# Kernel tuning notes

Hardware: AMD Instinct MI355X
Metric: run time of the kernel (lower is better)

## Reference

```python
import jax, jax.numpy as jnp
import numpy as np

N_NODES = 100000
N_EDGES = 1600000
N_FEAT = 128
HIDDEN = 128
N_GRAPHS = 100


def setup_inputs() -> dict:
    key = jax.random.key(0)
    ks = jax.random.split(key, 12)
    glorot = lambda k, fi, fo: jax.random.normal(k, (fo, fi), jnp.float32) * (1.0 / np.sqrt(fi))
    x = jax.random.normal(ks[0], (N_NODES, N_FEAT), jnp.float32)
    edge_index = jax.random.randint(ks[1], (2, N_EDGES), 0, N_NODES, jnp.int64)
    batch = jnp.sort(jax.random.randint(ks[2], (N_NODES,), 0, N_GRAPHS, jnp.int64))
    return {
        "x": x,
        "edge_index": edge_index,
        "batch": batch,
        "W1": glorot(ks[3], N_FEAT, HIDDEN), "b1": jnp.zeros((HIDDEN,), jnp.float32),
        "W2": glorot(ks[4], HIDDEN, HIDDEN), "b2": jnp.zeros((HIDDEN,), jnp.float32),
        "W3": glorot(ks[5], HIDDEN, HIDDEN), "b3": jnp.zeros((HIDDEN,), jnp.float32),
        "W4": glorot(ks[6], HIDDEN, HIDDEN), "b4": jnp.zeros((HIDDEN,), jnp.float32),
    }


def _aggregate(x, edge_index):
    # GIN aggregation with eps=0: (1+eps)*x_i + sum_{j in N(i)} x_j
    src, dst = edge_index[0], edge_index[1]
    agg = jax.ops.segment_sum(x[src], dst, num_segments=N_NODES)
    return x + agg


def _mlp(h, Wa, ba, Wb, bb):
    h = jax.nn.relu(h @ Wa.T + ba)
    return jax.nn.relu(h @ Wb.T + bb)


def reference(x, edge_index, batch, W1, b1, W2, b2, W3, b3, W4, b4):
    # conv1: GINConv(MLP1), then extra relu (no-op after MLP's relu), dropout in eval = identity
    h = _mlp(_aggregate(x, edge_index), W1, b1, W2, b2)
    # conv2: GINConv(MLP2), then relu
    h = _mlp(_aggregate(h, edge_index), W3, b3, W4, b4)
    # global mean pool over graphs
    sums = jax.ops.segment_sum(h, batch, num_segments=N_GRAPHS)
    counts = jax.ops.segment_sum(jnp.ones((h.shape[0],), h.dtype), batch, num_segments=N_GRAPHS)
    x_pool = sums / jnp.maximum(counts, 1.0)[:, None]
    return (x_pool, h)
```

## Files before the change

kernel.cpp:

```cpp
#include <hip/hip_runtime.h>

#define N_NODES  100000
#define N_EDGES  1600000
#define NF       128
#define N_GRAPHS 100
#define NBKT     391
#define BKT_SHIFT 8
#define CAP      6144
#define CAPN     48
#define EPB      4096
#define EB_GRID  391

typedef __attribute__((ext_vector_type(8))) short bf16x8;
typedef __attribute__((ext_vector_type(4))) float f32x4;
typedef __attribute__((ext_vector_type(2))) float f32x2;
typedef unsigned int uint32;

__device__ __forceinline__ unsigned short f2bf(float f) {
    union { float f; uint32 u; } x; x.f = f;
    return (unsigned short)((x.u + 0x7fffu + ((x.u >> 16) & 1u)) >> 16);
}
__device__ __forceinline__ uint32 pack2bf(float a, float b) {
    union { float f; uint32 u; } x, y; x.f = a; y.f = b;
    uint32 lo = (x.u + 0x7fffu + ((x.u >> 16) & 1u)) >> 16;
    uint32 hi = (y.u + 0x7fffu + ((y.u >> 16) & 1u)) & 0xffff0000u;
    return lo | hi;
}
__device__ __forceinline__ void add8(f32x2* acc, uint4 u4) {
    uint32 u[4] = {u4.x, u4.y, u4.z, u4.w};
    #pragma unroll
    for (int i = 0; i < 4; ++i) {
        union { uint32 b; float f; } lo, hi;
        lo.b = u[i] << 16; hi.b = u[i] & 0xffff0000u;
        acc[i] += (f32x2){lo.f, hi.f};
    }
}

__global__ __launch_bounds__(256) void prep(const float4* __restrict__ x,
                                            const float4* __restrict__ w1,
                                            const float4* __restrict__ w2,
                                            const float4* __restrict__ w3,
                                            const float4* __restrict__ w4,
                                            uint4* __restrict__ xb, uint4* __restrict__ wb,
                                            int* __restrict__ cur, float* __restrict__ sums) {
    int bid = blockIdx.x, t = threadIdx.x;
    if (bid < 6250) {
        int i = bid * 256 + t;
        float4 a = x[i * 2], b = x[i * 2 + 1];
        uint4 o;
        o.x = pack2bf(a.x, a.y); o.y = pack2bf(a.z, a.w);
        o.z = pack2bf(b.x, b.y); o.w = pack2bf(b.z, b.w);
        xb[i] = o;
    } else if (bid < 6282) {
        int i = (bid - 6250) * 256 + t;
        int wi = i >> 11, li = i & 2047;
        const float4* s = (wi == 0) ? w1 : (wi == 1) ? w2 : (wi == 2) ? w3 : w4;
        float4 a = s[li * 2], b = s[li * 2 + 1];
        uint4 o;
        o.x = pack2bf(a.x, a.y); o.y = pack2bf(a.z, a.w);
        o.z = pack2bf(b.x, b.y); o.w = pack2bf(b.z, b.w);
        wb[i] = o;
    } else {
        int idx = (bid - 6282) * 256 + t;
        for (int i = idx; i < N_GRAPHS * NF; i += 4096) sums[i] = 0.f;
        if (idx < NBKT) cur[idx] = 0;
    }
}

__global__ __launch_bounds__(512) void bscatter(const int* __restrict__ src,
                                                const int* __restrict__ dst,
                                                int* __restrict__ cur,
                                                uint32* __restrict__ ebuf) {
    __shared__ int lh[NBKT], lbase[NBKT];
    int t = threadIdx.x;
    if (t < NBKT) lh[t] = 0;
    __syncthreads();
    int e0 = blockIdx.x * EPB;
    int d[8];
    #pragma unroll
    for (int i = 0; i < 8; ++i) {
        int e = e0 + i * 512 + t;
        d[i] = -1;
        if (e < N_EDGES) { d[i] = dst[e]; atomicAdd(&lh[d[i] >> BKT_SHIFT], 1); }
    }
    __syncthreads();
    if (t < NBKT) { lbase[t] = t * CAP + atomicAdd(&cur[t], lh[t]); lh[t] = 0; }
    __syncthreads();
    #pragma unroll
    for (int i = 0; i < 8; ++i) {
        int e = e0 + i * 512 + t;
        if (e < N_EDGES) {
            int b = d[i] >> BKT_SHIFT;
            int off = atomicAdd(&lh[b], 1);
            ebuf[lbase[b] + off] = ((uint32)(d[i] & 255) << 17) | (uint32)src[e];
        }
    }
}

__global__ __launch_bounds__(256) void bfine(const uint32* __restrict__ ebuf,
                                             const int* __restrict__ cur,
                                             int* __restrict__ cnt,
                                             int* __restrict__ csr) {
    __shared__ int off[256];
    int t = threadIdx.x;
    int bkt = blockIdx.x;
    int beg = bkt * CAP;
    int end = beg + cur[bkt];
    off[t] = 0;
    __syncthreads();
    for (int e = beg + t; e < end; e += 256) {
        uint32 u = ebuf[e];
        int local = (int)(u >> 17);
        int pos = atomicAdd(&off[local], 1);
        if (pos < CAPN)
            csr[((bkt << BKT_SHIFT) + local) * CAPN + pos] = (int)(u & 0x1FFFFu);
    }
    __syncthreads();
    int node = (bkt << BKT_SHIFT) + t;
    if (node < N_NODES) cnt[node] = min(off[t], CAPN);
}

__global__ __launch_bounds__(256) void gather_agg_bf16(const uint4* __restrict__ x,
                                                       const int* __restrict__ cnt,
                                                       const int* __restrict__ csr,
                                                       uint4* __restrict__ out) {
    int gid  = blockIdx.x * 256 + threadIdx.x;
    int node = gid >> 6;
    int l = threadIdx.x & 63;
    int c = l & 15;
    int j = l >> 4;
    int beg = node * CAPN;

    uint4 vself = x[(size_t)node * 16 + c];
    int myE = csr[beg + min(l, CAPN - 1)];
    int deg = cnt[node];

    f32x2 acc[4];
    #pragma unroll
    for (int i = 0; i < 4; ++i) acc[i] = (f32x2){0.f, 0.f};

    uint4 v[8];
    int ok[8];
    #pragma unroll
    for (int k = 0; k < 4; ++k) {
        int sl = j + 4 * k;
        int sle = max(min(sl, deg - 1), 0);
        unsigned s = (unsigned)__shfl(myE, sle, 64);
        s = min(s, (unsigned)(N_NODES - 1));
        v[k] = x[(size_t)s * 16 + c];
        ok[k] = sl < deg;
    }
    if (deg > 16) {
        #pragma unroll
        for (int k = 0; k < 4; ++k) {
            int sl = 16 + j + 4 * k;
            int sle = min(sl, deg - 1);
            unsigned s = (unsigned)__shfl(myE, sle, 64);
            s = min(s, (unsigned)(N_NODES - 1));
            v[4 + k] = x[(size_t)s * 16 + c];
            ok[4 + k] = sl < deg;
        }
    }
    #pragma unroll
    for (int k = 0; k < 4; ++k) if (ok[k]) add8(acc, v[k]);
    if (deg > 16) {
        #pragma unroll
        for (int k = 0; k < 4; ++k) if (ok[4 + k]) add8(acc, v[4 + k]);
        for (int sl0 = 32; sl0 < deg; sl0 += 16) {
            #pragma unroll
            for (int k = 0; k < 4; ++k) {
                int sl = sl0 + j + 4 * k;
                int sle = min(sl, deg - 1);
                unsigned s = (unsigned)__shfl(myE, sle, 64);
                s = min(s, (unsigned)(N_NODES - 1));
                uint4 vv = x[(size_t)s * 16 + c];
                if (sl < deg) add8(acc, vv);
            }
        }
    }

    #pragma unroll
    for (int i = 0; i < 4; ++i) {
        acc[i].x += __shfl_xor(acc[i].x, 16, 64);
        acc[i].y += __shfl_xor(acc[i].y, 16, 64);
        acc[i].x += __shfl_xor(acc[i].x, 32, 64);
        acc[i].y += __shfl_xor(acc[i].y, 32, 64);
    }

    add8(acc, vself);

    if (j == 0) {
        uint4 o;
        o.x = pack2bf(acc[0].x, acc[0].y); o.y = pack2bf(acc[1].x, acc[1].y);
        o.z = pack2bf(acc[2].x, acc[2].y); o.w = pack2bf(acc[3].x, acc[3].y);
        out[(size_t)node * 16 + c] = o;
    }
}

template <bool F32OUT>
__global__ __launch_bounds__(256, 4) void mlp_mfma(const unsigned short* __restrict__ A,
                                                   const unsigned short* __restrict__ Wa,
                                                   const float* __restrict__ ba,
                                                   const unsigned short* __restrict__ Wb,
                                                   const float* __restrict__ bb,
                                                   void* __restrict__ Cout, int M) {
    __shared__ unsigned short Mid[128 * 136];
    int tid  = threadIdx.x;
    int row0 = blockIdx.x * 128;
    int wv = tid >> 6, l = tid & 63, lm = l & 15, q = l >> 4;

    const unsigned short* pa0 = A + (size_t)min(row0 + wv * 32 + lm,      M - 1) * NF;
    const unsigned short* pa1 = A + (size_t)min(row0 + wv * 32 + 16 + lm, M - 1) * NF;
    const unsigned short* pwa = Wa + lm * NF;
    const unsigned short* pwb = Wb + lm * NF;

    f32x4 acc[2][8];
    #pragma unroll
    for (int i = 0; i < 2; ++i)
        #pragma unroll
        for (int j = 0; j < 8; ++j) acc[i][j] = (f32x4){0.f, 0.f, 0.f, 0.f};

    #pragma unroll
    for (int ks = 0; ks < 4; ++ks) {
        int ko = ks * 32 + q * 8;
        bf16x8 a0 = *(const bf16x8*)(pa0 + ko);
        bf16x8 a1 = *(const bf16x8*)(pa1 + ko);
        #pragma unroll
        for (int ct = 0; ct < 8; ++ct) {
            bf16x8 b = *(const bf16x8*)(pwa + ct * 16 * NF + ko);
            acc[0][ct] = __builtin_amdgcn_mfma_f32_16x16x32_bf16(a0, b, acc[0][ct], 0, 0, 0);
            acc[1][ct] = __builtin_amdgcn_mfma_f32_16x16x32_bf16(a1, b, acc[1][ct], 0, 0, 0);
        }
    }

    #pragma unroll
    for (int rt = 0; rt < 2; ++rt)
        #pragma unroll
        for (int ct = 0; ct < 8; ++ct) {
            int col = ct * 16 + lm;
            float bv = ba[col];
            #pragma unroll
            for (int r = 0; r < 4; ++r) {
                int rr = wv * 32 + rt * 16 + q * 4 + r;
                Mid[rr * 136 + col] = f2bf(fmaxf(acc[rt][ct][r] + bv, 0.f));
            }
        }
    __syncthreads();

    #pragma unroll
    for (int i = 0; i < 2; ++i)
        #pragma unroll
        for (int j = 0; j < 8; ++j) acc[i][j] = (f32x4){0.f, 0.f, 0.f, 0.f};

    const unsigned short* pm0 = &Mid[(wv * 32 + lm) * 136];
    const unsigned short* pm1 = &Mid[(wv * 32 + 16 + lm) * 136];
    #pragma unroll
    for (int ks = 0; ks < 4; ++ks) {
        int ko = ks * 32 + q * 8;
        bf16x8 a0 = *(const bf16x8*)(pm0 + ko);
        bf16x8 a1 = *(const bf16x8*)(pm1 + ko);
        #pragma unroll
        for (int ct = 0; ct < 8; ++ct) {
            bf16x8 b = *(const bf16x8*)(pwb + ct * 16 * NF + ko);
            acc[0][ct] = __builtin_amdgcn_mfma_f32_16x16x32_bf16(a0, b, acc[0][ct], 0, 0, 0);
            acc[1][ct] = __builtin_amdgcn_mfma_f32_16x16x32_bf16(a1, b, acc[1][ct], 0, 0, 0);
        }
    }

    #pragma unroll
    for (int rt = 0; rt < 2; ++rt)
        #pragma unroll
        for (int ct = 0; ct < 8; ++ct) {
            int col = ct * 16 + lm;
            float bv = bb[col];
            #pragma unroll
            for (int r = 0; r < 4; ++r) {
                int row = row0 + wv * 32 + rt * 16 + q * 4 + r;
                if (row < M) {
                    float v = fmaxf(acc[rt][ct][r] + bv, 0.f);
                    if (F32OUT) ((float*)Cout)[(size_t)row * NF + col] = v;
                    else ((unsigned short*)Cout)[(size_t)row * NF + col] = f2bf(v);
                }
            }
        }
}

__global__ __launch_bounds__(256) void pool_sum2(const float* __restrict__ h,
                                                 const int* __restrict__ batch,
                                                 float* __restrict__ sums) {
    int t = threadIdx.x;
    int f = t & 127, seg = t >> 7;
    int n0 = blockIdx.x * 128 + seg * 64;
    if (n0 >= N_NODES) return;
    int n1 = min(n0 + 64, N_NODES);
    int cur = batch[n0];
    float acc = 0.f;
    for (int n = n0; n < n1; ++n) {
        int g = batch[n];
        if (g != cur) {
            atomicAdd(&sums[cur * NF + f], acc);
            acc = 0.f; cur = g;
        }
        acc += h[(size_t)n * NF + f];
    }
    atomicAdd(&sums[cur * NF + f], acc);
}

__global__ __launch_bounds__(256) void pool_div2(const float* __restrict__ sums,
                                                 const int* __restrict__ batch,
                                                 float* __restrict__ out) {
    int i = blockIdx.x * 256 + threadIdx.x;
    if (i >= N_GRAPHS * NF) return;
    int g = i >> 7;
    int lo = 0, hi = N_NODES;
    while (lo < hi) { int m = (lo + hi) >> 1; if (batch[m] < g) lo = m + 1; else hi = m; }
    int lo2 = lo, hi2 = N_NODES;
    while (lo2 < hi2) { int m = (lo2 + hi2) >> 1; if (batch[m] < g + 1) lo2 = m + 1; else hi2 = m; }
    float cnt = (float)(lo2 - lo);
    out[i] = sums[i] / fmaxf(cnt, 1.f);
}

extern "C" void kernel_launch(void* const* d_in, const int* in_sizes, int n_in,
                              void* d_out, int out_size, void* d_ws, size_t ws_size,
                              hipStream_t stream) {
    const float* x     = (const float*)d_in[0];
    const int*   ei    = (const int*)d_in[1];
    const int*   batch = (const int*)d_in[2];
    const float* W1 = (const float*)d_in[3];  const float* b1 = (const float*)d_in[4];
    const float* W2 = (const float*)d_in[5];  const float* b2 = (const float*)d_in[6];
    const float* W3 = (const float*)d_in[7];  const float* b3 = (const float*)d_in[8];
    const float* W4 = (const float*)d_in[9];  const float* b4 = (const float*)d_in[10];
    const int* src = ei;
    const int* dst = ei + N_EDGES;

    float* out   = (float*)d_out;
    float* h_out = out + N_GRAPHS * NF;

    const size_t NE = (size_t)N_NODES * NF;
    unsigned short* xb = (unsigned short*)d_ws;
    unsigned short* t0 = xb + NE;
    unsigned short* t1 = t0 + NE;
    unsigned short* Wb = t1 + NE;
    int*    csr  = (int*)(Wb + 4 * NF * NF);
    int*    cntp = csr + (size_t)N_NODES * CAPN;
    int*    curp = cntp + N_NODES;
    float*  sums = (float*)(curp + NBKT);
    uint32* ebuf = (uint32*)t1;

    const int gather_blocks = N_NODES * 64 / 256;
    const int gemm_blocks   = (N_NODES + 127) / 128;

    prep<<<6250 + 32 + 16, 256, 0, stream>>>((const float4*)x,
                                             (const float4*)W1, (const float4*)W2,
                                             (const float4*)W3, (const float4*)W4,
                                             (uint4*)xb, (uint4*)Wb, curp, sums);

    bscatter<<<EB_GRID, 512, 0, stream>>>(src, dst, curp, ebuf);
    bfine<<<NBKT, 256, 0, stream>>>(ebuf, curp, cntp, csr);

    gather_agg_bf16<<<gather_blocks, 256, 0, stream>>>((const uint4*)xb, cntp, csr, (uint4*)t0);
    mlp_mfma<false><<<gemm_blocks, 256, 0, stream>>>(t0, Wb + 0 * NF * NF, b1,
                                                     Wb + 1 * NF * NF, b2, t1, N_NODES);

    gather_agg_bf16<<<gather_blocks, 256, 0, stream>>>((const uint4*)t1, cntp, csr, (uint4*)t0);
    mlp_mfma<true ><<<gemm_blocks, 256, 0, stream>>>(t0, Wb + 2 * NF * NF, b3,
                                                     Wb + 3 * NF * NF, b4, h_out, N_NODES);

    pool_sum2<<<(N_NODES + 127) / 128, 256, 0, stream>>>(h_out, batch, sums);
    pool_div2<<<(N_GRAPHS * NF + 255) / 256, 256, 0, stream>>>(sums, batch, out);
}
```

Measured before the change: 394.7 us.

## Use persistent gather waves with prefetch and spread edge bucketing over more blocks

The gather kernel becomes persistent: a fixed grid of waves loops over nodes and prefetches the next node's CSR row and degree while the current node's neighbours are summed. The edge bucketing now uses smaller blocks (1024 edges each, so more blocks) and skips global atomics for empty buckets. The fine pass splits each bucket across four blocks and uses global atomics on per-node counters, which are now zeroed in prep, instead of a shared-memory histogram. This raises parallelism in the CSR build at the cost of more global atomic traffic. Degrees are clamped to CAPN when read in the gather.

New measurement: 473.9 us. 1.2x slower.

```diff
diff --git a/kernel.cpp b/kernel.cpp
--- a/kernel.cpp
+++ b/kernel.cpp
@@ -8,8 +8,10 @@
 #define BKT_SHIFT 8
 #define CAP      6144
 #define CAPN     48
-#define EPB      4096
-#define EB_GRID  391
+#define EPB      1024
+#define EB_GRID  1563
+#define GBLOCKS  2048
+#define NWAVES   (GBLOCKS * 4)
 
 typedef __attribute__((ext_vector_type(8))) short bf16x8;
 typedef __attribute__((ext_vector_type(4))) float f32x4;
@@ -42,7 +44,8 @@
                                             const float4* __restrict__ w3,
                                             const float4* __restrict__ w4,
                                             uint4* __restrict__ xb, uint4* __restrict__ wb,
-                                            int* __restrict__ cur, float* __restrict__ sums) {
+                                            int* __restrict__ cur, int* __restrict__ cnt,
+                                            float* __restrict__ sums) {
     int bid = blockIdx.x, t = threadIdx.x;
     if (bid < 6250) {
         int i = bid * 256 + t;
@@ -62,33 +65,38 @@
         wb[i] = o;
     } else {
         int idx = (bid - 6282) * 256 + t;
-        for (int i = idx; i < N_GRAPHS * NF; i += 4096) sums[i] = 0.f;
+        for (int i = idx; i < N_NODES; i += 8192) cnt[i] = 0;
+        for (int i = idx; i < N_GRAPHS * NF; i += 8192) sums[i] = 0.f;
         if (idx < NBKT) cur[idx] = 0;
     }
 }
 
-__global__ __launch_bounds__(512) void bscatter(const int* __restrict__ src,
+__global__ __launch_bounds__(256) void bscatter(const int* __restrict__ src,
                                                 const int* __restrict__ dst,
                                                 int* __restrict__ cur,
                                                 uint32* __restrict__ ebuf) {
     __shared__ int lh[NBKT], lbase[NBKT];
     int t = threadIdx.x;
-    if (t < NBKT) lh[t] = 0;
+    for (int i = t; i < NBKT; i += 256) lh[i] = 0;
     __syncthreads();
     int e0 = blockIdx.x * EPB;
-    int d[8];
-    #pragma unroll
-    for (int i = 0; i < 8; ++i) {
-        int e = e0 + i * 512 + t;
+    int d[4];
+    #pragma unroll
+    for (int i = 0; i < 4; ++i) {
+        int e = e0 + i * 256 + t;
         d[i] = -1;
         if (e < N_EDGES) { d[i] = dst[e]; atomicAdd(&lh[d[i] >> BKT_SHIFT], 1); }
     }
     __syncthreads();
-    if (t < NBKT) { lbase[t] = t * CAP + atomicAdd(&cur[t], lh[t]); lh[t] = 0; }
+    for (int i = t; i < NBKT; i += 256) {
+        int h = lh[i];
+        lbase[i] = i * CAP + (h ? atomicAdd(&cur[i], h) : 0);
+        lh[i] = 0;
+    }
     __syncthreads();
     #pragma unroll
-    for (int i = 0; i < 8; ++i) {
-        int e = e0 + i * 512 + t;
+    for (int i = 0; i < 4; ++i) {
+        int e = e0 + i * 256 + t;
         if (e < N_EDGES) {
             int b = d[i] >> BKT_SHIFT;
             int off = atomicAdd(&lh[b], 1);
@@ -101,99 +109,106 @@
                                              const int* __restrict__ cur,
                                              int* __restrict__ cnt,
                                              int* __restrict__ csr) {
-    __shared__ int off[256];
-    int t = threadIdx.x;
-    int bkt = blockIdx.x;
+    int bkt = blockIdx.x >> 2, q = blockIdx.x & 3;
     int beg = bkt * CAP;
-    int end = beg + cur[bkt];
-    off[t] = 0;
-    __syncthreads();
-    for (int e = beg + t; e < end; e += 256) {
+    int end = beg + min(cur[bkt], CAP);
+    int lo = beg + q * (CAP / 4);
+    int hi = min(lo + (CAP / 4), end);
+    for (int e = lo + (int)threadIdx.x; e < hi; e += 256) {
         uint32 u = ebuf[e];
-        int local = (int)(u >> 17);
-        int pos = atomicAdd(&off[local], 1);
+        int node = (bkt << BKT_SHIFT) + (int)(u >> 17);
+        int pos = atomicAdd(&cnt[node], 1);
         if (pos < CAPN)
-            csr[((bkt << BKT_SHIFT) + local) * CAPN + pos] = (int)(u & 0x1FFFFu);
-    }
-    __syncthreads();
-    int node = (bkt << BKT_SHIFT) + t;
-    if (node < N_NODES) cnt[node] = min(off[t], CAPN);
+            csr[node * CAPN + pos] = (int)(u & 0x1FFFFu);
+    }
 }
 
 __global__ __launch_bounds__(256) void gather_agg_bf16(const uint4* __restrict__ x,
                                                        const int* __restrict__ cnt,
                                                        const int* __restrict__ csr,
                                                        uint4* __restrict__ out) {
-    int gid  = blockIdx.x * 256 + threadIdx.x;
-    int node = gid >> 6;
+    int wid = (blockIdx.x * 256 + threadIdx.x) >> 6;
     int l = threadIdx.x & 63;
     int c = l & 15;
     int j = l >> 4;
-    int beg = node * CAPN;
-
-    uint4 vself = x[(size_t)node * 16 + c];
-    int myE = csr[beg + min(l, CAPN - 1)];
-    int deg = cnt[node];
-
-    f32x2 acc[4];
-    #pragma unroll
-    for (int i = 0; i < 4; ++i) acc[i] = (f32x2){0.f, 0.f};
-
-    uint4 v[8];
-    int ok[8];
-    #pragma unroll
-    for (int k = 0; k < 4; ++k) {
-        int sl = j + 4 * k;
-        int sle = max(min(sl, deg - 1), 0);
-        unsigned s = (unsigned)__shfl(myE, sle, 64);
-        s = min(s, (unsigned)(N_NODES - 1));
-        v[k] = x[(size_t)s * 16 + c];
-        ok[k] = sl < deg;
-    }
-    if (deg > 16) {
+    int le = min(l, CAPN - 1);
+
+    int node = wid;
+    int E  = csr[node * CAPN + le];
+    int dg = cnt[node];
+
+    while (node < N_NODES) {
+        int nn = node + NWAVES;
+        int deg = min(dg, CAPN);
+
+        uint4 vself = x[(size_t)node * 16 + c];
+
+        uint4 v[8];
         #pragma unroll
         for (int k = 0; k < 4; ++k) {
-            int sl = 16 + j + 4 * k;
-            int sle = min(sl, deg - 1);
-            unsigned s = (unsigned)__shfl(myE, sle, 64);
+            int sl = j + 4 * k;
+            int sle = max(min(sl, deg - 1), 0);
+            unsigned s = (unsigned)__shfl(E, sle, 64);
             s = min(s, (unsigned)(N_NODES - 1));
-            v[4 + k] = x[(size_t)s * 16 + c];
-            ok[4 + k] = sl < deg;
-        }
-    }
-    #pragma unroll
-    for (int k = 0; k < 4; ++k) if (ok[k]) add8(acc, v[k]);
-    if (deg > 16) {
-        #pragma unroll
-        for (int k = 0; k < 4; ++k) if (ok[4 + k]) add8(acc, v[4 + k]);
-        for (int sl0 = 32; sl0 < deg; sl0 += 16) {
+            v[k] = x[(size_t)s * 16 + c];
+        }
+        if (deg > 16) {
             #pragma unroll
             for (int k = 0; k < 4; ++k) {
-                int sl = sl0 + j + 4 * k;
+                int sl = 16 + j + 4 * k;
                 int sle = min(sl, deg - 1);
-                unsigned s = (unsigned)__shfl(myE, sle, 64);
+                unsigned s = (unsigned)__shfl(E, sle, 64);
                 s = min(s, (unsigned)(N_NODES - 1));
-                uint4 vv = x[(size_t)s * 16 + c];
-                if (sl < deg) add8(acc, vv);
+                v[4 + k] = x[(size_t)s * 16 + c];
             }
         }
-    }
-
-    #pragma unroll
-    for (int i = 0; i < 4; ++i) {
-        acc[i].x += __shfl_xor(acc[i].x, 16, 64);
-        acc[i].y += __shfl_xor(acc[i].y, 16, 64);
-        acc[i].x += __shfl_xor(acc[i].x, 32, 64);
-        acc[i].y += __shfl_xor(acc[i].y, 32, 64);
-    }
-
-    add8(acc, vself);
-
-    if (j == 0) {
-        uint4 o;
-        o.x = pack2bf(acc[0].x, acc[0].y); o.y = pack2bf(acc[1].x, acc[1].y);
-        o.z = pack2bf(acc[2].x, acc[2].y); o.w = pack2bf(acc[3].x, acc[3].y);
-        out[(size_t)node * 16 + c] = o;
+
+        int En = 0, dgn = 0;
+        if (nn < N_NODES) {
+            En  = csr[nn * CAPN + le];
+            dgn = cnt[nn];
+        }
+
+        f32x2 acc[4];
+        #pragma unroll
+        for (int i = 0; i < 4; ++i) acc[i] = (f32x2){0.f, 0.f};
+
+        #pragma unroll
+        for (int k = 0; k < 4; ++k) if (j + 4 * k < deg) add8(acc, v[k]);
+        if (deg > 16) {
+            #pragma unroll
+            for (int k = 0; k < 4; ++k) if (16 + j + 4 * k < deg) add8(acc, v[4 + k]);
+            for (int sl0 = 32; sl0 < deg; sl0 += 16) {
+                #pragma unroll
+                for (int k = 0; k < 4; ++k) {
+                    int sl = sl0 + j + 4 * k;
+                    int sle = min(sl, deg - 1);
+                    unsigned s = (unsigned)__shfl(E, sle, 64);
+                    s = min(s, (unsigned)(N_NODES - 1));
+                    uint4 vv = x[(size_t)s * 16 + c];
+                    if (sl < deg) add8(acc, vv);
+                }
+            }
+        }
+
+        #pragma unroll
+        for (int i = 0; i < 4; ++i) {
+            acc[i].x += __shfl_xor(acc[i].x, 16, 64);
+            acc[i].y += __shfl_xor(acc[i].y, 16, 64);
+            acc[i].x += __shfl_xor(acc[i].x, 32, 64);
+            acc[i].y += __shfl_xor(acc[i].y, 32, 64);
+        }
+
+        add8(acc, vself);
+
+        if (j == 0) {
+            uint4 o;
+            o.x = pack2bf(acc[0].x, acc[0].y); o.y = pack2bf(acc[1].x, acc[1].y);
+            o.z = pack2bf(acc[2].x, acc[2].y); o.w = pack2bf(acc[3].x, acc[3].y);
+            out[(size_t)node * 16 + c] = o;
+        }
+
+        node = nn; E = En; dg = dgn;
     }
 }
 
@@ -347,22 +362,21 @@
     float*  sums = (float*)(curp + NBKT);
     uint32* ebuf = (uint32*)t1;
 
-    const int gather_blocks = N_NODES * 64 / 256;
-    const int gemm_blocks   = (N_NODES + 127) / 128;
-
-    prep<<<6250 + 32 + 16, 256, 0, stream>>>((const float4*)x,
+    const int gemm_blocks = (N_NODES + 127) / 128;
+
+    prep<<<6250 + 32 + 32, 256, 0, stream>>>((const float4*)x,
                                              (const float4*)W1, (const float4*)W2,
                                              (const float4*)W3, (const float4*)W4,
-                                             (uint4*)xb, (uint4*)Wb, curp, sums);
-
-    bscatter<<<EB_GRID, 512, 0, stream>>>(src, dst, curp, ebuf);
-    bfine<<<NBKT, 256, 0, stream>>>(ebuf, curp, cntp, csr);
-
-    gather_agg_bf16<<<gather_blocks, 256, 0, stream>>>((const uint4*)xb, cntp, csr, (uint4*)t0);
+                                             (uint4*)xb, (uint4*)Wb, curp, cntp, sums);
+
+    bscatter<<<EB_GRID, 256, 0, stream>>>(src, dst, curp, ebuf);
+    bfine<<<NBKT * 4, 256, 0, stream>>>(ebuf, curp, cntp, csr);
+
+    gather_agg_bf16<<<GBLOCKS, 256, 0, stream>>>((const uint4*)xb, cntp, csr, (uint4*)t0);
     mlp_mfma<false><<<gemm_blocks, 256, 0, stream>>>(t0, Wb + 0 * NF * NF, b1,
                                                      Wb + 1 * NF * NF, b2, t1, N_NODES);
 
-    gather_agg_bf16<<<gather_blocks, 256, 0, stream>>>((const uint4*)t1, cntp, csr, (uint4*)t0);
+    gather_agg_bf16<<<GBLOCKS, 256, 0, stream>>>((const uint4*)t1, cntp, csr, (uint4*)t0);
     mlp_mfma<true ><<<gemm_blocks, 256, 0, stream>>>(t0, Wb + 2 * NF * NF, b3,
                                                      Wb + 3 * NF * NF, b4, h_out, N_NODES);
 
```

## Split gather/MLP stages so MLP on first part overlaps gather of remainder

Applied to the files above, without the earlier changes.

Each GIN layer's gather and MLP are split at a node boundary. The first gather covers the first part of the nodes. A fused kernel then runs MLP blocks on that part alongside gather blocks for the rest, and a final MLP launch finishes the tail, so compute-bound GEMM overlaps memory-bound gather. bfine also stages its CSR rows in shared memory and writes them out as coalesced uint4 copies, and pool_sum now uses float4 loads. The cost is a large shared-memory buffer in bfine that lowers its occupancy, plus an extra kernel launch per layer.

Result: slower. 404.4 us (+2.5%).

```diff
diff --git a/kernel.cpp b/kernel.cpp
--- a/kernel.cpp
+++ b/kernel.cpp
@@ -10,6 +10,12 @@
 #define CAPN     48
 #define EPB      4096
 #define EB_GRID  391
+#define HSPLIT   66560
+#define MBLK_A   520
+#define GNODES_B (N_NODES - HSPLIT)
+#define GBLK_B   (GNODES_B / 4)
+#define GBLK_A   (HSPLIT / 4)
+#define MBLK_B   262
 
 typedef __attribute__((ext_vector_type(8))) short bf16x8;
 typedef __attribute__((ext_vector_type(4))) float f32x4;
@@ -102,10 +108,11 @@
                                              int* __restrict__ cnt,
                                              int* __restrict__ csr) {
     __shared__ int off[256];
+    __shared__ __align__(16) int lcsr[256 * CAPN];
     int t = threadIdx.x;
     int bkt = blockIdx.x;
     int beg = bkt * CAP;
-    int end = beg + cur[bkt];
+    int end = beg + min(cur[bkt], CAP);
     off[t] = 0;
     __syncthreads();
     for (int e = beg + t; e < end; e += 256) {
@@ -113,22 +120,22 @@
         int local = (int)(u >> 17);
         int pos = atomicAdd(&off[local], 1);
         if (pos < CAPN)
-            csr[((bkt << BKT_SHIFT) + local) * CAPN + pos] = (int)(u & 0x1FFFFu);
+            lcsr[local * CAPN + pos] = (int)(u & 0x1FFFFu);
     }
     __syncthreads();
     int node = (bkt << BKT_SHIFT) + t;
     if (node < N_NODES) cnt[node] = min(off[t], CAPN);
-}
-
-__global__ __launch_bounds__(256) void gather_agg_bf16(const uint4* __restrict__ x,
-                                                       const int* __restrict__ cnt,
-                                                       const int* __restrict__ csr,
-                                                       uint4* __restrict__ out) {
-    int gid  = blockIdx.x * 256 + threadIdx.x;
-    int node = gid >> 6;
-    int l = threadIdx.x & 63;
-    int c = l & 15;
-    int j = l >> 4;
+    uint4* dstq = (uint4*)(csr + (size_t)bkt * 256 * CAPN);
+    const uint4* srcq = (const uint4*)lcsr;
+    for (int i = t; i < 256 * CAPN / 4; i += 256)
+        dstq[i] = srcq[i];
+}
+
+__device__ __forceinline__ void gather_one(const uint4* __restrict__ x,
+                                           const int* __restrict__ cnt,
+                                           const int* __restrict__ csr,
+                                           uint4* __restrict__ out,
+                                           int node, int l, int c, int j) {
     int beg = node * CAPN;
 
     uint4 vself = x[(size_t)node * 16 + c];
@@ -197,16 +204,26 @@
     }
 }
 
+__global__ __launch_bounds__(256) void gather_agg_bf16(const uint4* __restrict__ x,
+                                                       const int* __restrict__ cnt,
+                                                       const int* __restrict__ csr,
+                                                       uint4* __restrict__ out,
+                                                       int g0) {
+    int gid  = blockIdx.x * 256 + threadIdx.x;
+    int node = g0 + (gid >> 6);
+    int l = threadIdx.x & 63;
+    gather_one(x, cnt, csr, out, node, l, l & 15, l >> 4);
+}
+
 template <bool F32OUT>
-__global__ __launch_bounds__(256, 4) void mlp_mfma(const unsigned short* __restrict__ A,
-                                                   const unsigned short* __restrict__ Wa,
-                                                   const float* __restrict__ ba,
-                                                   const unsigned short* __restrict__ Wb,
-                                                   const float* __restrict__ bb,
-                                                   void* __restrict__ Cout, int M) {
+__device__ __forceinline__ void mlp_body(const unsigned short* __restrict__ A,
+                                         const unsigned short* __restrict__ Wa,
+                                         const float* __restrict__ ba,
+                                         const unsigned short* __restrict__ Wb,
+                                         const float* __restrict__ bb,
+                                         void* __restrict__ Cout, int M, int row0) {
     __shared__ unsigned short Mid[128 * 136];
     int tid  = threadIdx.x;
-    int row0 = blockIdx.x * 128;
     int wv = tid >> 6, l = tid & 63, lm = l & 15, q = l >> 4;
 
     const unsigned short* pa0 = A + (size_t)min(row0 + wv * 32 + lm,      M - 1) * NF;
@@ -285,25 +302,63 @@
         }
 }
 
-__global__ __launch_bounds__(256) void pool_sum2(const float* __restrict__ h,
+template <bool F32OUT>
+__global__ __launch_bounds__(256, 4) void mlp_mfma(const unsigned short* __restrict__ A,
+                                                   const unsigned short* __restrict__ Wa,
+                                                   const float* __restrict__ ba,
+                                                   const unsigned short* __restrict__ Wb,
+                                                   const float* __restrict__ bb,
+                                                   void* __restrict__ Cout, int M, int rowBase) {
+    mlp_body<F32OUT>(A, Wa, ba, Wb, bb, Cout, M, rowBase + blockIdx.x * 128);
+}
+
+template <bool F32OUT>
+__global__ __launch_bounds__(256, 4) void fused_mg(const unsigned short* __restrict__ A,
+                                                   const unsigned short* __restrict__ Wa,
+                                                   const float* __restrict__ ba,
+                                                   const unsigned short* __restrict__ Wb,
+                                                   const float* __restrict__ bb,
+                                                   void* __restrict__ Cout,
+                                                   const uint4* __restrict__ gx,
+                                                   const int* __restrict__ cnt,
+                                                   const int* __restrict__ csr,
+                                                   uint4* __restrict__ gout) {
+    if (blockIdx.x < MBLK_A) {
+        mlp_body<F32OUT>(A, Wa, ba, Wb, bb, Cout, HSPLIT, blockIdx.x * 128);
+    } else {
+        int idx = (blockIdx.x - MBLK_A) * 256 + threadIdx.x;
+        int node = HSPLIT + (idx >> 6);
+        int l = threadIdx.x & 63;
+        gather_one(gx, cnt, csr, gout, node, l, l & 15, l >> 4);
+    }
+}
+
+__global__ __launch_bounds__(256) void pool_sum4(const float4* __restrict__ h,
                                                  const int* __restrict__ batch,
                                                  float* __restrict__ sums) {
     int t = threadIdx.x;
-    int f = t & 127, seg = t >> 7;
-    int n0 = blockIdx.x * 128 + seg * 64;
+    int f4 = t & 31, seg = t >> 5;
+    int n0 = blockIdx.x * 512 + seg * 64;
     if (n0 >= N_NODES) return;
     int n1 = min(n0 + 64, N_NODES);
     int cur = batch[n0];
-    float acc = 0.f;
+    float4 acc = {0.f, 0.f, 0.f, 0.f};
     for (int n = n0; n < n1; ++n) {
         int g = batch[n];
         if (g != cur) {
-            atomicAdd(&sums[cur * NF + f], acc);
-            acc = 0.f; cur = g;
-        }
-        acc += h[(size_t)n * NF + f];
-    }
-    atomicAdd(&sums[cur * NF + f], acc);
+            atomicAdd(&sums[cur * NF + f4 * 4 + 0], acc.x);
+            atomicAdd(&sums[cur * NF + f4 * 4 + 1], acc.y);
+            atomicAdd(&sums[cur * NF + f4 * 4 + 2], acc.z);
+            atomicAdd(&sums[cur * NF + f4 * 4 + 3], acc.w);
+            acc = (float4){0.f, 0.f, 0.f, 0.f}; cur = g;
+        }
+        float4 v = h[(size_t)n * 32 + f4];
+        acc.x += v.x; acc.y += v.y; acc.z += v.z; acc.w += v.w;
+    }
+    atomicAdd(&sums[cur * NF + f4 * 4 + 0], acc.x);
+    atomicAdd(&sums[cur * NF + f4 * 4 + 1], acc.y);
+    atomicAdd(&sums[cur * NF + f4 * 4 + 2], acc.z);
+    atomicAdd(&sums[cur * NF + f4 * 4 + 3], acc.w);
 }
 
 __global__ __launch_bounds__(256) void pool_div2(const float* __restrict__ sums,
@@ -337,18 +392,16 @@
     float* h_out = out + N_GRAPHS * NF;
 
     const size_t NE = (size_t)N_NODES * NF;
+    const size_t CSRSZ = (size_t)NBKT * 256 * CAPN;
     unsigned short* xb = (unsigned short*)d_ws;
     unsigned short* t0 = xb + NE;
     unsigned short* t1 = t0 + NE;
     unsigned short* Wb = t1 + NE;
     int*    csr  = (int*)(Wb + 4 * NF * NF);
-    int*    cntp = csr + (size_t)N_NODES * CAPN;
+    int*    cntp = csr + CSRSZ;
     int*    curp = cntp + N_NODES;
     float*  sums = (float*)(curp + NBKT);
     uint32* ebuf = (uint32*)t1;
-
-    const int gather_blocks = N_NODES * 64 / 256;
-    const int gemm_blocks   = (N_NODES + 127) / 128;
 
     prep<<<6250 + 32 + 16, 256, 0, stream>>>((const float4*)x,
                                              (const float4*)W1, (const float4*)W2,
@@ -358,14 +411,20 @@
     bscatter<<<EB_GRID, 512, 0, stream>>>(src, dst, curp, ebuf);
     bfine<<<NBKT, 256, 0, stream>>>(ebuf, curp, cntp, csr);
 
-    gather_agg_bf16<<<gather_blocks, 256, 0, stream>>>((const uint4*)xb, cntp, csr, (uint4*)t0);
-    mlp_mfma<false><<<gemm_blocks, 256, 0, stream>>>(t0, Wb + 0 * NF * NF, b1,
-                                                     Wb + 1 * NF * NF, b2, t1, N_NODES);
-
-    gather_agg_bf16<<<gather_blocks, 256, 0, stream>>>((const uint4*)t1, cntp, csr, (uint4*)t0);
-    mlp_mfma<true ><<<gemm_blocks, 256, 0, stream>>>(t0, Wb + 2 * NF * NF, b3,
-                                                     Wb + 3 * NF * NF, b4, h_out, N_NODES);
-
-    pool_sum2<<<(N_NODES + 127) / 128, 256, 0, stream>>>(h_out, batch, sums);
+    gather_agg_bf16<<<GBLK_A, 256, 0, stream>>>((const uint4*)xb, cntp, csr, (uint4*)t0, 0);
+    fused_mg<false><<<MBLK_A + GBLK_B, 256, 0, stream>>>(t0, Wb + 0 * NF * NF, b1,
+                                                         Wb + 1 * NF * NF, b2, t1,
+                                                         (const uint4*)xb, cntp, csr, (uint4*)t0);
+    mlp_mfma<false><<<MBLK_B, 256, 0, stream>>>(t0, Wb + 0 * NF * NF, b1,
+                                                Wb + 1 * NF * NF, b2, t1, N_NODES, HSPLIT);
+
+    gather_agg_bf16<<<GBLK_A, 256, 0, stream>>>((const uint4*)t1, cntp, csr, (uint4*)t0, 0);
+    fused_mg<true ><<<MBLK_A + GBLK_B, 256, 0, stream>>>(t0, Wb + 2 * NF * NF, b3,
+                                                         Wb + 3 * NF * NF, b4, h_out,
+                                                         (const uint4*)t1, cntp, csr, (uint4*)t0);
+    mlp_mfma<true ><<<MBLK_B, 256, 0, stream>>>(t0, Wb + 2 * NF * NF, b3,
+                                                Wb + 3 * NF * NF, b4, h_out, N_NODES, HSPLIT);
+
+    pool_sum4<<<(N_NODES + 511) / 512, 256, 0, stream>>>((const float4*)h_out, batch, sums);
     pool_div2<<<(N_GRAPHS * NF + 255) / 256, 256, 0, stream>>>(sums, batch, out);
 }
```

## Fuse neighbor gather with MFMA MLP and stage CSR build in LDS

Applied to the files above, without the earlier changes.

Replaces the separate gather-aggregate and MLP kernels with one 512-thread kernel per 128-row tile. It aggregates neighbor features straight into LDS and runs both MFMA GEMMs from there. This removes the bf16 intermediate buffer round trip through global memory and one launch per layer. It also builds each bucket's CSR in LDS before a coalesced copy-out, skips zero-count global atomics in bscatter, and vectorizes the pool sum with float4. The cost is less parallelism in the gather, since each wave walks 16 nodes serially, plus higher LDS use per block, which may lower occupancy and latency hiding for the random loads.

Result: slower. 467.3 us (+18.4%).

```diff
diff --git a/kernel.cpp b/kernel.cpp
--- a/kernel.cpp
+++ b/kernel.cpp
@@ -10,6 +10,7 @@
 #define CAPN     48
 #define EPB      4096
 #define EB_GRID  391
+#define FBLOCKS  782
 
 typedef __attribute__((ext_vector_type(8))) short bf16x8;
 typedef __attribute__((ext_vector_type(4))) float f32x4;
@@ -84,7 +85,7 @@
         if (e < N_EDGES) { d[i] = dst[e]; atomicAdd(&lh[d[i] >> BKT_SHIFT], 1); }
     }
     __syncthreads();
-    if (t < NBKT) { lbase[t] = t * CAP + atomicAdd(&cur[t], lh[t]); lh[t] = 0; }
+    if (t < NBKT) { lbase[t] = t * CAP + (lh[t] ? atomicAdd(&cur[t], lh[t]) : 0); lh[t] = 0; }
     __syncthreads();
     #pragma unroll
     for (int i = 0; i < 8; ++i) {
@@ -102,10 +103,11 @@
                                              int* __restrict__ cnt,
                                              int* __restrict__ csr) {
     __shared__ int off[256];
+    __shared__ __align__(16) int lcsr[256 * CAPN];
     int t = threadIdx.x;
     int bkt = blockIdx.x;
     int beg = bkt * CAP;
-    int end = beg + cur[bkt];
+    int end = beg + min(cur[bkt], CAP);
     off[t] = 0;
     __syncthreads();
     for (int e = beg + t; e < end; e += 256) {
@@ -113,197 +115,195 @@
         int local = (int)(u >> 17);
         int pos = atomicAdd(&off[local], 1);
         if (pos < CAPN)
-            csr[((bkt << BKT_SHIFT) + local) * CAPN + pos] = (int)(u & 0x1FFFFu);
+            lcsr[local * CAPN + pos] = (int)(u & 0x1FFFFu);
     }
     __syncthreads();
     int node = (bkt << BKT_SHIFT) + t;
     if (node < N_NODES) cnt[node] = min(off[t], CAPN);
-}
-
-__global__ __launch_bounds__(256) void gather_agg_bf16(const uint4* __restrict__ x,
-                                                       const int* __restrict__ cnt,
-                                                       const int* __restrict__ csr,
-                                                       uint4* __restrict__ out) {
-    int gid  = blockIdx.x * 256 + threadIdx.x;
-    int node = gid >> 6;
-    int l = threadIdx.x & 63;
+    uint4* dstq = (uint4*)(csr + (size_t)bkt * 256 * CAPN);
+    const uint4* srcq = (const uint4*)lcsr;
+    for (int i = t; i < 256 * CAPN / 4; i += 256)
+        dstq[i] = srcq[i];
+}
+
+template <bool F32OUT>
+__global__ __launch_bounds__(512) void fused_gml(const uint4* __restrict__ x,
+                                                 const int* __restrict__ cnt,
+                                                 const int* __restrict__ csr,
+                                                 const unsigned short* __restrict__ Wa,
+                                                 const float* __restrict__ ba,
+                                                 const unsigned short* __restrict__ Wb,
+                                                 const float* __restrict__ bb,
+                                                 void* __restrict__ Cout) {
+    __shared__ __align__(16) unsigned short AM[128 * 136];
+    int tid = threadIdx.x;
+    int wv = tid >> 6;
+    int l  = tid & 63;
     int c = l & 15;
     int j = l >> 4;
-    int beg = node * CAPN;
-
-    uint4 vself = x[(size_t)node * 16 + c];
-    int myE = csr[beg + min(l, CAPN - 1)];
-    int deg = cnt[node];
-
-    f32x2 acc[4];
-    #pragma unroll
-    for (int i = 0; i < 4; ++i) acc[i] = (f32x2){0.f, 0.f};
-
-    uint4 v[8];
-    int ok[8];
-    #pragma unroll
-    for (int k = 0; k < 4; ++k) {
-        int sl = j + 4 * k;
-        int sle = max(min(sl, deg - 1), 0);
-        unsigned s = (unsigned)__shfl(myE, sle, 64);
-        s = min(s, (unsigned)(N_NODES - 1));
-        v[k] = x[(size_t)s * 16 + c];
-        ok[k] = sl < deg;
-    }
-    if (deg > 16) {
+    int row0 = blockIdx.x * 128;
+
+    for (int i = 0; i < 16; ++i) {
+        int lrow = wv * 16 + i;
+        int node = min(row0 + lrow, N_NODES - 1);
+        int beg = node * CAPN;
+
+        uint4 vself = x[(size_t)node * 16 + c];
+        int myE = csr[beg + min(l, CAPN - 1)];
+        int deg = cnt[node];
+
+        f32x2 acc[4];
+        #pragma unroll
+        for (int a = 0; a < 4; ++a) acc[a] = (f32x2){0.f, 0.f};
+
+        uint4 v[8];
+        int ok[8];
         #pragma unroll
         for (int k = 0; k < 4; ++k) {
-            int sl = 16 + j + 4 * k;
-            int sle = min(sl, deg - 1);
+            int sl = j + 4 * k;
+            int sle = max(min(sl, deg - 1), 0);
             unsigned s = (unsigned)__shfl(myE, sle, 64);
             s = min(s, (unsigned)(N_NODES - 1));
-            v[4 + k] = x[(size_t)s * 16 + c];
-            ok[4 + k] = sl < deg;
-        }
-    }
-    #pragma unroll
-    for (int k = 0; k < 4; ++k) if (ok[k]) add8(acc, v[k]);
-    if (deg > 16) {
-        #pragma unroll
-        for (int k = 0; k < 4; ++k) if (ok[4 + k]) add8(acc, v[4 + k]);
-        for (int sl0 = 32; sl0 < deg; sl0 += 16) {
+            v[k] = x[(size_t)s * 16 + c];
+            ok[k] = sl < deg;
+        }
+        if (deg > 16) {
             #pragma unroll
             for (int k = 0; k < 4; ++k) {
-                int sl = sl0 + j + 4 * k;
+                int sl = 16 + j + 4 * k;
                 int sle = min(sl, deg - 1);
                 unsigned s = (unsigned)__shfl(myE, sle, 64);
                 s = min(s, (unsigned)(N_NODES - 1));
-                uint4 vv = x[(size_t)s * 16 + c];
-                if (sl < deg) add8(acc, vv);
+                v[4 + k] = x[(size_t)s * 16 + c];
+                ok[4 + k] = sl < deg;
             }
         }
-    }
-
-    #pragma unroll
-    for (int i = 0; i < 4; ++i) {
-        acc[i].x += __shfl_xor(acc[i].x, 16, 64);
-        acc[i].y += __shfl_xor(acc[i].y, 16, 64);
-        acc[i].x += __shfl_xor(acc[i].x, 32, 64);
-        acc[i].y += __shfl_xor(acc[i].y, 32, 64);
-    }
-
-    add8(acc, vself);
-
-    if (j == 0) {
-        uint4 o;
-        o.x = pack2bf(acc[0].x, acc[0].y); o.y = pack2bf(acc[1].x, acc[1].y);
-        o.z = pack2bf(acc[2].x, acc[2].y); o.w = pack2bf(acc[3].x, acc[3].y);
-        out[(size_t)node * 16 + c] = o;
-    }
-}
-
-template <bool F32OUT>
-__global__ __launch_bounds__(256, 4) void mlp_mfma(const unsigned short* __restrict__ A,
-                                                   const unsigned short* __restrict__ Wa,
-                                                   const float* __restrict__ ba,
-                                                   const unsigned short* __restrict__ Wb,
-                                                   const float* __restrict__ bb,
-                                                   void* __restrict__ Cout, int M) {
-    __shared__ unsigned short Mid[128 * 136];
-    int tid  = threadIdx.x;
-    int row0 = blockIdx.x * 128;
-    int wv = tid >> 6, l = tid & 63, lm = l & 15, q = l >> 4;
-
-    const unsigned short* pa0 = A + (size_t)min(row0 + wv * 32 + lm,      M - 1) * NF;
-    const unsigned short* pa1 = A + (size_t)min(row0 + wv * 32 + 16 + lm, M - 1) * NF;
+        #pragma unroll
+        for (int k = 0; k < 4; ++k) if (ok[k]) add8(acc, v[k]);
+        if (deg > 16) {
+            #pragma unroll
+            for (int k = 0; k < 4; ++k) if (ok[4 + k]) add8(acc, v[4 + k]);
+            for (int sl0 = 32; sl0 < deg; sl0 += 16) {
+                #pragma unroll
+                for (int k = 0; k < 4; ++k) {
+                    int sl = sl0 + j + 4 * k;
+                    int sle = min(sl, deg - 1);
+                    unsigned s = (unsigned)__shfl(myE, sle, 64);
+                    s = min(s, (unsigned)(N_NODES - 1));
+                    uint4 vv = x[(size_t)s * 16 + c];
+                    if (sl < deg) add8(acc, vv);
+                }
+            }
+        }
+
+        #pragma unroll
+        for (int a = 0; a < 4; ++a) {
+            acc[a].x += __shfl_xor(acc[a].x, 16, 64);
+            acc[a].y += __shfl_xor(acc[a].y, 16, 64);
+            acc[a].x += __shfl_xor(acc[a].x, 32, 64);
+            acc[a].y += __shfl_xor(acc[a].y, 32, 64);
+        }
+
+        add8(acc, vself);
+
+        if (j == 0) {
+            uint4 o;
+            o.x = pack2bf(acc[0].x, acc[0].y); o.y = pack2bf(acc[1].x, acc[1].y);
+            o.z = pack2bf(acc[2].x, acc[2].y); o.w = pack2bf(acc[3].x, acc[3].y);
+            *(uint4*)&AM[lrow * 136 + c * 8] = o;
+        }
+    }
+    __syncthreads();
+
+    int lm = c, q = j;
+    const unsigned short* pa  = &AM[(wv * 16 + lm) * 136];
     const unsigned short* pwa = Wa + lm * NF;
     const unsigned short* pwb = Wb + lm * NF;
 
-    f32x4 acc[2][8];
-    #pragma unroll
-    for (int i = 0; i < 2; ++i)
-        #pragma unroll
-        for (int j = 0; j < 8; ++j) acc[i][j] = (f32x4){0.f, 0.f, 0.f, 0.f};
+    f32x4 acc[8];
+    #pragma unroll
+    for (int ct = 0; ct < 8; ++ct) acc[ct] = (f32x4){0.f, 0.f, 0.f, 0.f};
 
     #pragma unroll
     for (int ks = 0; ks < 4; ++ks) {
         int ko = ks * 32 + q * 8;
-        bf16x8 a0 = *(const bf16x8*)(pa0 + ko);
-        bf16x8 a1 = *(const bf16x8*)(pa1 + ko);
+        bf16x8 a = *(const bf16x8*)(pa + ko);
         #pragma unroll
         for (int ct = 0; ct < 8; ++ct) {
             bf16x8 b = *(const bf16x8*)(pwa + ct * 16 * NF + ko);
-            acc[0][ct] = __builtin_amdgcn_mfma_f32_16x16x32_bf16(a0, b, acc[0][ct], 0, 0, 0);
-            acc[1][ct] = __builtin_amdgcn_mfma_f32_16x16x32_bf16(a1, b, acc[1][ct], 0, 0, 0);
-        }
-    }
-
-    #pragma unroll
-    for (int rt = 0; rt < 2; ++rt)
-        #pragma unroll
-        for (int ct = 0; ct < 8; ++ct) {
-            int col = ct * 16 + lm;
-            float bv = ba[col];
-            #pragma unroll
-            for (int r = 0; r < 4; ++r) {
-                int rr = wv * 32 + rt * 16 + q * 4 + r;
-                Mid[rr * 136 + col] = f2bf(fmaxf(acc[rt][ct][r] + bv, 0.f));
-            }
-        }
-    __syncthreads();
-
-    #pragma unroll
-    for (int i = 0; i < 2; ++i)
-        #pragma unroll
-        for (int j = 0; j < 8; ++j) acc[i][j] = (f32x4){0.f, 0.f, 0.f, 0.f};
-
-    const unsigned short* pm0 = &Mid[(wv * 32 + lm) * 136];
-    const unsigned short* pm1 = &Mid[(wv * 32 + 16 + lm) * 136];
+            acc[ct] = __builtin_amdgcn_mfma_f32_16x16x32_bf16(a, b, acc[ct], 0, 0, 0);
+        }
+    }
+    __syncthreads();
+
+    #pragma unroll
+    for (int ct = 0; ct < 8; ++ct) {
+        int col = ct * 16 + lm;
+        float bv = ba[col];
+        #pragma unroll
+        for (int r = 0; r < 4; ++r) {
+            int rr = wv * 16 + q * 4 + r;
+            AM[rr * 136 + col] = f2bf(fmaxf(acc[ct][r] + bv, 0.f));
+        }
+    }
+    __syncthreads();
+
+    #pragma unroll
+    for (int ct = 0; ct < 8; ++ct) acc[ct] = (f32x4){0.f, 0.f, 0.f, 0.f};
+
     #pragma unroll
     for (int ks = 0; ks < 4; ++ks) {
         int ko = ks * 32 + q * 8;
-        bf16x8 a0 = *(const bf16x8*)(pm0 + ko);
-        bf16x8 a1 = *(const bf16x8*)(pm1 + ko);
+        bf16x8 a = *(const bf16x8*)(pa + ko);
         #pragma unroll
         for (int ct = 0; ct < 8; ++ct) {
             bf16x8 b = *(const bf16x8*)(pwb + ct * 16 * NF + ko);
-            acc[0][ct] = __builtin_amdgcn_mfma_f32_16x16x32_bf16(a0, b, acc[0][ct], 0, 0, 0);
-            acc[1][ct] = __builtin_amdgcn_mfma_f32_16x16x32_bf16(a1, b, acc[1][ct], 0, 0, 0);
-        }
-    }
-
-    #pragma unroll
-    for (int rt = 0; rt < 2; ++rt)
-        #pragma unroll
-        for (int ct = 0; ct < 8; ++ct) {
-            int col = ct * 16 + lm;
-            float bv = bb[col];
-            #pragma unroll
-            for (int r = 0; r < 4; ++r) {
-                int row = row0 + wv * 32 + rt * 16 + q * 4 + r;
-                if (row < M) {
-                    float v = fmaxf(acc[rt][ct][r] + bv, 0.f);
-                    if (F32OUT) ((float*)Cout)[(size_t)row * NF + col] = v;
-                    else ((unsigned short*)Cout)[(size_t)row * NF + col] = f2bf(v);
-                }
+            acc[ct] = __builtin_amdgcn_mfma_f32_16x16x32_bf16(a, b, acc[ct], 0, 0, 0);
+        }
+    }
+
+    #pragma unroll
+    for (int ct = 0; ct < 8; ++ct) {
+        int col = ct * 16 + lm;
+        float bv = bb[col];
+        #pragma unroll
+        for (int r = 0; r < 4; ++r) {
+            int row = row0 + wv * 16 + q * 4 + r;
+            if (row < N_NODES) {
+                float vv = fmaxf(acc[ct][r] + bv, 0.f);
+                if (F32OUT) ((float*)Cout)[(size_t)row * NF + col] = vv;
+                else ((unsigned short*)Cout)[(size_t)row * NF + col] = f2bf(vv);
             }
         }
-}
-
-__global__ __launch_bounds__(256) void pool_sum2(const float* __restrict__ h,
+    }
+}
+
+__global__ __launch_bounds__(256) void pool_sum4(const float4* __restrict__ h,
                                                  const int* __restrict__ batch,
                                                  float* __restrict__ sums) {
     int t = threadIdx.x;
-    int f = t & 127, seg = t >> 7;
-    int n0 = blockIdx.x * 128 + seg * 64;
+    int f4 = t & 31, seg = t >> 5;
+    int n0 = blockIdx.x * 128 + seg * 16;
     if (n0 >= N_NODES) return;
-    int n1 = min(n0 + 64, N_NODES);
+    int n1 = min(n0 + 16, N_NODES);
     int cur = batch[n0];
-    float acc = 0.f;
+    float4 acc = {0.f, 0.f, 0.f, 0.f};
     for (int n = n0; n < n1; ++n) {
         int g = batch[n];
         if (g != cur) {
-            atomicAdd(&sums[cur * NF + f], acc);
-            acc = 0.f; cur = g;
-        }
-        acc += h[(size_t)n * NF + f];
-    }
-    atomicAdd(&sums[cur * NF + f], acc);
+            atomicAdd(&sums[cur * NF + f4 * 4 + 0], acc.x);
+            atomicAdd(&sums[cur * NF + f4 * 4 + 1], acc.y);
+            atomicAdd(&sums[cur * NF + f4 * 4 + 2], acc.z);
+            atomicAdd(&sums[cur * NF + f4 * 4 + 3], acc.w);
+            acc = (float4){0.f, 0.f, 0.f, 0.f}; cur = g;
+        }
+        float4 v = h[(size_t)n * 32 + f4];
+        acc.x += v.x; acc.y += v.y; acc.z += v.z; acc.w += v.w;
+    }
+    atomicAdd(&sums[cur * NF + f4 * 4 + 0], acc.x);
+    atomicAdd(&sums[cur * NF + f4 * 4 + 1], acc.y);
+    atomicAdd(&sums[cur * NF + f4 * 4 + 2], acc.z);
+    atomicAdd(&sums[cur * NF + f4 * 4 + 3], acc.w);
 }
 
 __global__ __launch_bounds__(256) void pool_div2(const float* __restrict__ sums,
@@ -338,17 +338,13 @@
 
     const size_t NE = (size_t)N_NODES * NF;
     unsigned short* xb = (unsigned short*)d_ws;
-    unsigned short* t0 = xb + NE;
-    unsigned short* t1 = t0 + NE;
+    unsigned short* t1 = xb + NE;
     unsigned short* Wb = t1 + NE;
     int*    csr  = (int*)(Wb + 4 * NF * NF);
-    int*    cntp = csr + (size_t)N_NODES * CAPN;
+    int*    cntp = csr + (size_t)NBKT * 256 * CAPN;
     int*    curp = cntp + N_NODES;
     float*  sums = (float*)(curp + NBKT);
     uint32* ebuf = (uint32*)t1;
-
-    const int gather_blocks = N_NODES * 64 / 256;
-    const int gemm_blocks   = (N_NODES + 127) / 128;
 
     prep<<<6250 + 32 + 16, 256, 0, stream>>>((const float4*)x,
                                              (const float4*)W1, (const float4*)W2,
@@ -358,14 +354,14 @@
     bscatter<<<EB_GRID, 512, 0, stream>>>(src, dst, curp, ebuf);
     bfine<<<NBKT, 256, 0, stream>>>(ebuf, curp, cntp, csr);
 
-    gather_agg_bf16<<<gather_blocks, 256, 0, stream>>>((const uint4*)xb, cntp, csr, (uint4*)t0);
-    mlp_mfma<false><<<gemm_blocks, 256, 0, stream>>>(t0, Wb + 0 * NF * NF, b1,
-                                                     Wb + 1 * NF * NF, b2, t1, N_NODES);
-
-    gather_agg_bf16<<<gather_blocks, 256, 0, stream>>>((const uint4*)t1, cntp, csr, (uint4*)t0);
-    mlp_mfma<true ><<<gemm_blocks, 256, 0, stream>>>(t0, Wb + 2 * NF * NF, b3,
-                                                     Wb + 3 * NF * NF, b4, h_out, N_NODES);
-
-    pool_sum2<<<(N_NODES + 127) / 128, 256, 0, stream>>>(h_out, batch, sums);
+    fused_gml<false><<<FBLOCKS, 512, 0, stream>>>((const uint4*)xb, cntp, csr,
+                                                  Wb + 0 * NF * NF, b1,
+                                                  Wb + 1 * NF * NF, b2, t1);
+
+    fused_gml<true ><<<FBLOCKS, 512, 0, stream>>>((const uint4*)t1, cntp, csr,
+                                                  Wb + 2 * NF * NF, b3,
+                                                  Wb + 3 * NF * NF, b4, h_out);
+
+    pool_sum4<<<(N_NODES + 127) / 128, 256, 0, stream>>>((const float4*)h_out, batch, sums);
     pool_div2<<<(N_GRAPHS * NF + 255) / 256, 256, 0, stream>>>(sums, batch, out);
 }
```
